# Optimization experiments

Hardware: AMD Instinct MI355X
Metric: run time of the kernel (lower is better)

The kernel has to match this reference:

```python
import jax, jax.numpy as jnp
import numpy as np

N_NODES = 50000
N_EDGES = 500000
HID = 128
NLAYERS = 4
NGRAPHS = 64
NODE_F = 15
EDGE_F = 3


def _init(key, shape, fan_in):
    return jax.random.normal(key, shape, dtype=jnp.float32) / np.sqrt(fan_in)


def setup_inputs() -> dict:
    key = jax.random.key(0)
    ks = jax.random.split(key, 32)
    inp = {}
    inp["x"] = jax.random.normal(ks[0], (N_NODES, NODE_F), dtype=jnp.float32)
    inp["edge_index"] = jax.random.randint(ks[1], (2, N_EDGES), 0, N_NODES, dtype=jnp.int64)
    inp["edge_attr"] = jax.random.normal(ks[2], (N_EDGES, EDGE_F), dtype=jnp.float32)
    inp["pos"] = jax.random.normal(ks[3], (N_NODES, 3), dtype=jnp.float32)
    inp["batch"] = jnp.sort(jax.random.randint(ks[4], (N_NODES,), 0, NGRAPHS, dtype=jnp.int64))
    # encoders
    inp["enc_w"] = _init(ks[5], (NODE_F, HID), NODE_F)
    inp["enc_b"] = jnp.zeros((HID,), jnp.float32)
    inp["eenc_w"] = _init(ks[6], (EDGE_F, HID), EDGE_F)
    inp["eenc_b"] = jnp.zeros((HID,), jnp.float32)
    # stacked per-layer conv params
    MIN = 2 * HID + 1  # message input dim = 257
    inp["msg_w1"] = _init(ks[7], (NLAYERS, MIN, HID), MIN)
    inp["msg_b1"] = jnp.zeros((NLAYERS, HID), jnp.float32)
    inp["msg_w2"] = _init(ks[8], (NLAYERS, HID, HID), HID)
    inp["msg_b2"] = jnp.zeros((NLAYERS, HID), jnp.float32)
    inp["upd_w1"] = _init(ks[9], (NLAYERS, 2 * HID, HID), 2 * HID)
    inp["upd_b1"] = jnp.zeros((NLAYERS, HID), jnp.float32)
    inp["upd_w2"] = _init(ks[10], (NLAYERS, HID, HID), HID)
    inp["upd_b2"] = jnp.zeros((NLAYERS, HID), jnp.float32)
    inp["ln_g"] = jnp.ones((NLAYERS, HID), jnp.float32)
    inp["ln_b"] = jnp.zeros((NLAYERS, HID), jnp.float32)
    # readout MLP (dropout is eval-mode identity)
    inp["mlp_w1"] = _init(ks[11], (HID, HID), HID)
    inp["mlp_b1"] = jnp.zeros((HID,), jnp.float32)
    inp["mlp_w2"] = _init(ks[12], (HID, HID // 2), HID)
    inp["mlp_b2"] = jnp.zeros((HID // 2,), jnp.float32)
    inp["mlp_w3"] = _init(ks[13], (HID // 2, 1), HID // 2)
    inp["mlp_b3"] = jnp.zeros((1,), jnp.float32)
    return inp


def reference(x, edge_index, edge_attr, pos, batch,
              enc_w, enc_b, eenc_w, eenc_b,
              msg_w1, msg_b1, msg_w2, msg_b2,
              upd_w1, upd_b1, upd_w2, upd_b2,
              ln_g, ln_b,
              mlp_w1, mlp_b1, mlp_w2, mlp_b2, mlp_w3, mlp_b3):
    n = x.shape[0]
    h = x @ enc_w + enc_b                      # [N, H] node encoder
    _ea = edge_attr @ eenc_w + eenc_b          # encoded but unused downstream (faithful to source)
    src = edge_index[0]                        # j (source)
    dst = edge_index[1]                        # i (target)
    dist = jnp.linalg.norm(pos[dst] - pos[src], axis=-1, keepdims=True)  # [E,1]
    for i in range(NLAYERS):
        xi = h[dst]
        xj = h[src]
        m_in = jnp.concatenate([xi, xj, dist], axis=-1)               # [E, 2H+1]
        m = jax.nn.relu(m_in @ msg_w1[i] + msg_b1[i]) @ msg_w2[i] + msg_b2[i]
        aggr = jax.ops.segment_sum(m, dst, num_segments=n)            # scatter-add -> [N,H]
        u_in = jnp.concatenate([h, aggr], axis=-1)                    # [N, 2H]
        u = jax.nn.relu(u_in @ upd_w1[i] + upd_b1[i]) @ upd_w2[i] + upd_b2[i]
        mu = jnp.mean(u, axis=-1, keepdims=True)
        var = jnp.mean((u - mu) ** 2, axis=-1, keepdims=True)
        u = (u - mu) / jnp.sqrt(var + 1e-5) * ln_g[i] + ln_b[i]
        u = jax.nn.relu(u)
        h = u if i == 0 else h + u
    # global mean pool over graphs
    cnt = jax.ops.segment_sum(jnp.ones((n, 1), h.dtype), batch, num_segments=NGRAPHS)
    pooled = jax.ops.segment_sum(h, batch, num_segments=NGRAPHS) / jnp.maximum(cnt, 1.0)
    o = jax.nn.relu(pooled @ mlp_w1 + mlp_b1)
    o = jax.nn.relu(o @ mlp_w2 + mlp_b2)
    return o @ mlp_w3 + mlp_b3                  # [NGRAPHS, 1]
```

## Files before the change

kernel.cpp:

```cpp
#include <hip/hip_runtime.h>
#include <hip/hip_bf16.h>
#include <cstdint>

#define N_NODES 50000
#define N_EDGES 500000
#define HID 128
#define NLAYERS 4
#define NGRAPHS 64
#define NTILES ((N_NODES + 63) / 64)
#define NPW 4
#define EBLOCKS ((N_NODES + NPW * 4 - 1) / (NPW * 4))

typedef float f32x4 __attribute__((ext_vector_type(4)));
typedef __bf16 bf16x8 __attribute__((ext_vector_type(8)));

__device__ float          g_h[(size_t)N_NODES * HID];
__device__ unsigned short g_hb[(size_t)N_NODES * HID];
__device__ float          g_S[(size_t)N_NODES * HID];
__device__ unsigned short g_PQ[(size_t)N_NODES * 256];
__device__ int2           g_edge[N_EDGES];
__device__ int            g_cnt[N_NODES];
__device__ int            g_cursor[N_NODES];
__device__ int            g_bsum[1024];
__device__ unsigned short g_pqw[NLAYERS * 4 * 16 * 64 * 8];
__device__ float          g_wc[NLAYERS * 128 * 128];
__device__ float          g_bc[NLAYERS * 128];
__device__ unsigned short g_uw1p[NLAYERS * 8 * 8 * 64 * 8];
__device__ unsigned short g_uw2p[NLAYERS * 4 * 8 * 64 * 8];
__device__ float          g_pooled[NGRAPHS * HID];

__device__ __forceinline__ unsigned short f2bf(float f) {
    uint32_t u = __builtin_bit_cast(uint32_t, f);
    uint32_t r = (u + 0x7fffu + ((u >> 16) & 1u)) >> 16;
    return (unsigned short)r;
}
__device__ __forceinline__ float bf2f(unsigned short u) {
    return __builtin_bit_cast(float, (uint32_t)u << 16);
}

__global__ void clear_cnt_k() {
    int i = blockIdx.x * 256 + threadIdx.x;
    if (i < N_NODES) g_cnt[i] = 0;
}
__global__ void clear_pooled_k() {
    int i = blockIdx.x * 256 + threadIdx.x;
    if (i < NGRAPHS * HID) g_pooled[i] = 0.f;
}

__global__ void pack_pqw_k(const float* __restrict__ w1) {
    int lane = threadIdx.x;
    int bid = blockIdx.x;
    int nt = bid & 15, ks = (bid >> 4) & 3, L = bid >> 6;
    const float* w = w1 + (size_t)L * 257 * HID;
    int kb = ks * 32 + (lane >> 4) * 8;
    int n = nt * 16 + (lane & 15);
    unsigned short tmp[8];
#pragma unroll
    for (int j = 0; j < 8; ++j) {
        int k = kb + j;
        float v = (n < 128) ? w[(size_t)k * HID + n] : w[(size_t)(128 + k) * HID + (n - 128)];
        tmp[j] = f2bf(v);
    }
    uint4 o = make_uint4(tmp[0] | ((uint32_t)tmp[1] << 16), tmp[2] | ((uint32_t)tmp[3] << 16),
                         tmp[4] | ((uint32_t)tmp[5] << 16), tmp[6] | ((uint32_t)tmp[7] << 16));
    *(uint4*)&g_pqw[(((size_t)(L * 4 + ks) * 16 + nt) * 64 + lane) * 8] = o;
}

__global__ void wc_k(const float* __restrict__ mw2, const float* __restrict__ uw1) {
    __shared__ float row[128];
    int L = blockIdx.x >> 7, k = blockIdx.x & 127, j = threadIdx.x;
    row[j] = mw2[(size_t)L * 128 * 128 + k * 128 + j];
    __syncthreads();
    const float* u1b = uw1 + (size_t)L * 256 * 128 + 128 * 128;
    float s = 0.f;
    for (int i = 0; i < 128; ++i) s += row[i] * u1b[i * 128 + j];
    g_wc[(size_t)L * 128 * 128 + k * 128 + j] = s;
}
__global__ void bc_k(const float* __restrict__ mb2, const float* __restrict__ uw1) {
    int L = blockIdx.x, j = threadIdx.x;
    const float* u1b = uw1 + (size_t)L * 256 * 128 + 128 * 128;
    const float* b2 = mb2 + L * 128;
    float s = 0.f;
    for (int i = 0; i < 128; ++i) s += b2[i] * u1b[i * 128 + j];
    g_bc[L * 128 + j] = s;
}

__global__ void pack_u1_k(const float* __restrict__ uw1) {
    int lane = threadIdx.x;
    int bid = blockIdx.x;
    int nt = bid & 7, ks = (bid >> 3) & 7, L = bid >> 6;
    int kb = ks * 32 + (lane >> 4) * 8;
    int n = nt * 16 + (lane & 15);
    unsigned short tmp[8];
#pragma unroll
    for (int j = 0; j < 8; ++j) {
        int k = kb + j;
        float v = (k < 128) ? uw1[(size_t)L * 256 * 128 + (size_t)k * 128 + n]
                            : g_wc[(size_t)L * 128 * 128 + (size_t)(k - 128) * 128 + n];
        tmp[j] = f2bf(v);
    }
    uint4 o = make_uint4(tmp[0] | ((uint32_t)tmp[1] << 16), tmp[2] | ((uint32_t)tmp[3] << 16),
                         tmp[4] | ((uint32_t)tmp[5] << 16), tmp[6] | ((uint32_t)tmp[7] << 16));
    *(uint4*)&g_uw1p[(((size_t)(L * 8 + ks) * 8 + nt) * 64 + lane) * 8] = o;
}

__global__ void pack_w2_k(const float* __restrict__ uw2) {
    int lane = threadIdx.x;
    int bid = blockIdx.x;
    int nt = bid & 7, ks = (bid >> 3) & 3, L = bid >> 5;
    int kb = ks * 32 + (lane >> 4) * 8;
    int n = nt * 16 + (lane & 15);
    unsigned short tmp[8];
#pragma unroll
    for (int j = 0; j < 8; ++j)
        tmp[j] = f2bf(uw2[(size_t)L * 128 * 128 + (size_t)(kb + j) * 128 + n]);
    uint4 o = make_uint4(tmp[0] | ((uint32_t)tmp[1] << 16), tmp[2] | ((uint32_t)tmp[3] << 16),
                         tmp[4] | ((uint32_t)tmp[5] << 16), tmp[6] | ((uint32_t)tmp[7] << 16));
    *(uint4*)&g_uw2p[(((size_t)(L * 4 + ks) * 8 + nt) * 64 + lane) * 8] = o;
}

__global__ void encode_k(const float* __restrict__ x, const float* __restrict__ w,
                         const float* __restrict__ b) {
    __shared__ float xl[2][15];
    int t = threadIdx.x;
    int half = t >> 7;
    int node = blockIdx.x * 2 + half;
    int c = t & 127;
    if (c < 15) xl[half][c] = x[(size_t)node * 15 + c];
    __syncthreads();
    float acc = b[c];
#pragma unroll
    for (int k = 0; k < 15; ++k) acc += xl[half][k] * w[k * HID + c];
    g_h[(size_t)node * HID + c] = acc;
    g_hb[(size_t)node * HID + c] = f2bf(acc);
}

__global__ void hist_k(const int* __restrict__ ei) {
    int e = blockIdx.x * 256 + threadIdx.x;
    if (e < N_EDGES) atomicAdd(&g_cnt[ei[N_EDGES + e]], 1);
}
__global__ void scanA_k() {
    __shared__ int s[512];
    int t = threadIdx.x;
    int i = blockIdx.x * 512 + t;
    s[t] = (i < N_NODES) ? g_cnt[i] : 0;
    __syncthreads();
    for (int d = 256; d > 0; d >>= 1) {
        if (t < d) s[t] += s[t + d];
        __syncthreads();
    }
    if (t == 0) g_bsum[blockIdx.x] = s[0];
}
__global__ void scanB_k(int nb) {
    if (threadIdx.x == 0) {
        int acc = 0;
        for (int i = 0; i < nb; ++i) { int v = g_bsum[i]; g_bsum[i] = acc; acc += v; }
    }
}
__global__ void scanC_k() {
    __shared__ int s[512];
    int t = threadIdx.x;
    int i = blockIdx.x * 512 + t;
    int v = (i < N_NODES) ? g_cnt[i] : 0;
    s[t] = v;
    __syncthreads();
    for (int d = 1; d < 512; d <<= 1) {
        int add = (t >= d) ? s[t - d] : 0;
        __syncthreads();
        s[t] += add;
        __syncthreads();
    }
    if (i < N_NODES) g_cursor[i] = g_bsum[blockIdx.x] + s[t] - v;
}
__global__ void scatter_k(const int* __restrict__ ei, const float* __restrict__ pos) {
    int e = blockIdx.x * 256 + threadIdx.x;
    if (e >= N_EDGES) return;
    int s = ei[e];
    int d = ei[N_EDGES + e];
    float dx = pos[d * 3 + 0] - pos[s * 3 + 0];
    float dy = pos[d * 3 + 1] - pos[s * 3 + 1];
    float dz = pos[d * 3 + 2] - pos[s * 3 + 2];
    float dist = sqrtf(dx * dx + dy * dy + dz * dz);
    int p = atomicAdd(&g_cursor[d], 1);
    g_edge[p] = make_int2(s, __builtin_bit_cast(int, dist));
}

__global__ __launch_bounds__(256, 2)
void pq_k(int L) {
    __shared__ unsigned short Abuf[64 * 128];
    __shared__ unsigned short Obuf[64 * 264];
    const unsigned short* wp = g_pqw + (size_t)L * 4 * 16 * 64 * 8;
    int t = threadIdx.x, wave = t >> 6, lane = t & 63;
    int arow = lane & 15, kgrp = lane >> 4;
    int tile0 = blockIdx.x * 64;

    {
        int r = t >> 2, p = t & 3;
        int n = tile0 + r;
        bool valid = n < N_NODES;
#pragma unroll
        for (int q = 0; q < 4; ++q) {
            int slot = p * 4 + q;
            uint4 v = make_uint4(0, 0, 0, 0);
            if (valid) v = *(const uint4*)&g_hb[(size_t)n * HID + slot * 8];
            *(uint4*)&Abuf[r * 128 + ((slot ^ (r & 7)) << 3)] = v;
        }
    }
    __syncthreads();

    bf16x8 wv[4][4];
#pragma unroll
    for (int ks = 0; ks < 4; ++ks)
#pragma unroll
        for (int ntl = 0; ntl < 4; ++ntl)
            wv[ks][ntl] = *(const bf16x8*)&wp[((size_t)(ks * 16 + wave * 4 + ntl) * 64 + lane) * 8];

    f32x4 acc[4][4];
#pragma unroll
    for (int rf = 0; rf < 4; ++rf)
#pragma unroll
        for (int ntl = 0; ntl < 4; ++ntl) acc[rf][ntl] = (f32x4){0.f, 0.f, 0.f, 0.f};
#pragma unroll
    for (int ks = 0; ks < 4; ++ks) {
        int slot = ks * 4 + kgrp;
#pragma unroll
        for (int rf = 0; rf < 4; ++rf) {
            int row = rf * 16 + arow;
            bf16x8 a = *(const bf16x8*)&Abuf[row * 128 + ((slot ^ (row & 7)) << 3)];
#pragma unroll
            for (int ntl = 0; ntl < 4; ++ntl)
                acc[rf][ntl] = __builtin_amdgcn_mfma_f32_16x16x32_bf16(a, wv[ks][ntl], acc[rf][ntl], 0, 0, 0);
        }
    }
#pragma unroll
    for (int rf = 0; rf < 4; ++rf)
#pragma unroll
        for (int ntl = 0; ntl < 4; ++ntl) {
            int col = wave * 64 + ntl * 16 + arow;
#pragma unroll
            for (int q = 0; q < 4; ++q) {
                int row = rf * 16 + kgrp * 4 + q;
                Obuf[row * 264 + col] = f2bf(acc[rf][ntl][q]);
            }
        }
    __syncthreads();
#pragma unroll
    for (int i = 0; i < 8; ++i) {
        int k = t + i * 256;
        int row = k >> 5, cc = k & 31;
        int n = tile0 + row;
        if (n < N_NODES)
            *(uint4*)&g_PQ[(size_t)n * 256 + cc * 8] = *(const uint4*)&Obuf[row * 264 + cc * 8];
    }
}

__global__ __launch_bounds__(256, 8)
void edge_relu_k(const float* __restrict__ w1last, const float* __restrict__ b1) {
    int t = threadIdx.x, wave = t >> 6, lane = t & 63;
    int c2 = lane * 2;
    float wl0 = w1last[c2], wl1 = w1last[c2 + 1];
    float bb0 = b1[c2], bb1 = b1[c2 + 1];

    int gw = blockIdx.x * 4 + wave;
    int n0 = gw * NPW;
    int n1 = n0 + NPW < N_NODES ? n0 + NPW : N_NODES;

    for (int n = n0; n < n1; ++n) {
        int end = g_cursor[n];
        int cnt = g_cnt[n];
        int beg = end - cnt;
        uint32_t pv = *(const uint32_t*)&g_PQ[(size_t)n * 256 + c2];
        float pb0 = bf2f((unsigned short)(pv & 0xffff)) + bb0;
        float pb1 = bf2f((unsigned short)(pv >> 16)) + bb1;
        float acc0 = 0.f, acc1 = 0.f;

        for (int cb = beg; cb < end; cb += 64) {
            int mye = cb + lane;
            bool v = mye < end;
            int2 ed = v ? g_edge[mye] : make_int2(0, 0);
            int msrc = ed.x;
            float mdist = __builtin_bit_cast(float, ed.y);
            int lim = end - cb < 64 ? end - cb : 64;
            int full = lim & ~7;
            for (int b = 0; b < full; b += 8) {
                uint32_t qv[8];
#pragma unroll
                for (int j = 0; j < 8; ++j) {
                    int s = __shfl(msrc, b + j);
                    qv[j] = *(const uint32_t*)&g_PQ[(size_t)s * 256 + 128 + c2];
                }
#pragma unroll
                for (int j = 0; j < 8; ++j) {
                    float dist = __shfl(mdist, b + j);
                    acc0 += fmaxf(fmaf(dist, wl0, pb0 + bf2f((unsigned short)(qv[j] & 0xffff))), 0.f);
                    acc1 += fmaxf(fmaf(dist, wl1, pb1 + bf2f((unsigned short)(qv[j] >> 16))), 0.f);
                }
            }
            for (int j = full; j < lim; ++j) {
                int s = __shfl(msrc, j);
                float dist = __shfl(mdist, j);
                uint32_t qv = *(const uint32_t*)&g_PQ[(size_t)s * 256 + 128 + c2];
                acc0 += fmaxf(fmaf(dist, wl0, pb0 + bf2f((unsigned short)(qv & 0xffff))), 0.f);
                acc1 += fmaxf(fmaf(dist, wl1, pb1 + bf2f((unsigned short)(qv >> 16))), 0.f);
            }
        }
        *(float2*)&g_S[(size_t)n * HID + c2] = make_float2(acc0, acc1);
    }
}

__global__ __launch_bounds__(256, 4)
void upd_k(const float* __restrict__ ub1, const float* __restrict__ ub2,
           const float* __restrict__ lng, const float* __restrict__ lnb,
           int L, int first_layer, int Lpq) {
    __shared__ unsigned short Abuf[64 * 128];
    __shared__ unsigned short Hbuf[64 * 128];
    __shared__ float rsums[2][2][64];
    __shared__ float degb[64];
    const unsigned short* w1p = g_uw1p + (size_t)L * 8 * 8 * 64 * 8;
    const unsigned short* w2p = g_uw2p + (size_t)L * 4 * 8 * 64 * 8;
    int t = threadIdx.x, wave = t >> 6, lane = t & 63;
    int wr = wave >> 1, wc = wave & 1;
    int arow = lane & 15, kgrp = lane >> 4;
    int tile0 = blockIdx.x * 64;

    int sr = t >> 2, sp = t & 3;
    int sn = tile0 + sr;
    bool svalid = sn < N_NODES;

    if (sp == 0) degb[sr] = svalid ? (float)g_cnt[sn] : 0.f;
#pragma unroll
    for (int q = 0; q < 4; ++q) {
        int slot = sp * 4 + q;
        uint4 v = make_uint4(0, 0, 0, 0);
        if (svalid) v = *(const uint4*)&g_hb[(size_t)sn * HID + slot * 8];
        *(uint4*)&Abuf[sr * 128 + ((slot ^ (sr & 7)) << 3)] = v;
    }
    __syncthreads();

    f32x4 acc0[4], acc1[4];
#pragma unroll
    for (int i = 0; i < 4; ++i) { acc0[i] = (f32x4){0.f,0.f,0.f,0.f}; acc1[i] = (f32x4){0.f,0.f,0.f,0.f}; }
    int r0 = wr * 32 + arow, r1 = r0 + 16;
#pragma unroll
    for (int ks = 0; ks < 4; ++ks) {
        int slot = ks * 4 + kgrp;
        bf16x8 a0 = *(const bf16x8*)&Abuf[r0 * 128 + ((slot ^ (arow & 7)) << 3)];
        bf16x8 a1 = *(const bf16x8*)&Abuf[r1 * 128 + ((slot ^ (arow & 7)) << 3)];
#pragma unroll
        for (int ntl = 0; ntl < 4; ++ntl) {
            bf16x8 b = *(const bf16x8*)&w1p[((size_t)(ks * 8 + wc * 4 + ntl) * 64 + lane) * 8];
            acc0[ntl] = __builtin_amdgcn_mfma_f32_16x16x32_bf16(a0, b, acc0[ntl], 0, 0, 0);
            acc1[ntl] = __builtin_amdgcn_mfma_f32_16x16x32_bf16(a1, b, acc1[ntl], 0, 0, 0);
        }
    }
    __syncthreads();

#pragma unroll
    for (int q = 0; q < 4; ++q) {
        int slot = sp * 4 + q;
        uint4 v = make_uint4(0, 0, 0, 0);
        if (svalid) {
            const float* spt = &g_S[(size_t)sn * HID + slot * 8];
            float4 f0 = *(const float4*)spt;
            float4 f1 = *((const float4*)spt + 1);
            v.x = f2bf(f0.x) | ((uint32_t)f2bf(f0.y) << 16);
            v.y = f2bf(f0.z) | ((uint32_t)f2bf(f0.w) << 16);
            v.z = f2bf(f1.x) | ((uint32_t)f2bf(f1.y) << 16);
            v.w = f2bf(f1.z) | ((uint32_t)f2bf(f1.w) << 16);
        }
        *(uint4*)&Abuf[sr * 128 + ((slot ^ (sr & 7)) << 3)] = v;
    }
    __syncthreads();

#pragma unroll
    for (int ks = 0; ks < 4; ++ks) {
        int slot = ks * 4 + kgrp;
        bf16x8 a0 = *(const bf16x8*)&Abuf[r0 * 128 + ((slot ^ (arow & 7)) << 3)];
        bf16x8 a1 = *(const bf16x8*)&Abuf[r1 * 128 + ((slot ^ (arow & 7)) << 3)];
#pragma unroll
        for (int ntl = 0; ntl < 4; ++ntl) {
            bf16x8 b = *(const bf16x8*)&w1p[((size_t)((ks + 4) * 8 + wc * 4 + ntl) * 64 + lane) * 8];
            acc0[ntl] = __builtin_amdgcn_mfma_f32_16x16x32_bf16(a0, b, acc0[ntl], 0, 0, 0);
            acc1[ntl] = __builtin_amdgcn_mfma_f32_16x16x32_bf16(a1, b, acc1[ntl], 0, 0, 0);
        }
    }

    float dg0[4], dg1[4];
#pragma unroll
    for (int q = 0; q < 4; ++q) {
        dg0[q] = degb[wr * 32 + kgrp * 4 + q];
        dg1[q] = degb[wr * 32 + 16 + kgrp * 4 + q];
    }
#pragma unroll
    for (int ntl = 0; ntl < 4; ++ntl) {
        int col = wc * 64 + ntl * 16 + arow;
        float bv1 = ub1[col], bcv = g_bc[L * 128 + col];
        int slotH = col >> 3, cl = col & 7;
#pragma unroll
        for (int q = 0; q < 4; ++q) {
            int rw0 = wr * 32 + kgrp * 4 + q;
            float h0 = fmaxf(acc0[ntl][q] + dg0[q] * bcv + bv1, 0.f);
            Hbuf[rw0 * 128 + ((slotH ^ (rw0 & 7)) << 3) + cl] = f2bf(h0);
            int rw1 = rw0 + 16;
            float h1 = fmaxf(acc1[ntl][q] + dg1[q] * bcv + bv1, 0.f);
            Hbuf[rw1 * 128 + ((slotH ^ (rw1 & 7)) << 3) + cl] = f2bf(h1);
        }
    }
    __syncthreads();

    f32x4 c0[4], c1[4];
#pragma unroll
    for (int i = 0; i < 4; ++i) { c0[i] = (f32x4){0.f,0.f,0.f,0.f}; c1[i] = (f32x4){0.f,0.f,0.f,0.f}; }
#pragma unroll
    for (int ks = 0; ks < 4; ++ks) {
        int slot = ks * 4 + kgrp;
        bf16x8 a0 = *(const bf16x8*)&Hbuf[r0 * 128 + ((slot ^ (arow & 7)) << 3)];
        bf16x8 a1 = *(const bf16x8*)&Hbuf[r1 * 128 + ((slot ^ (arow & 7)) << 3)];
#pragma unroll
        for (int ntl = 0; ntl < 4; ++ntl) {
            bf16x8 b = *(const bf16x8*)&w2p[((size_t)(ks * 8 + wc * 4 + ntl) * 64 + lane) * 8];
            c0[ntl] = __builtin_amdgcn_mfma_f32_16x16x32_bf16(a0, b, c0[ntl], 0, 0, 0);
            c1[ntl] = __builtin_amdgcn_mfma_f32_16x16x32_bf16(a1, b, c1[ntl], 0, 0, 0);
        }
    }

    float bv2[4], gm[4], bt[4];
#pragma unroll
    for (int ntl = 0; ntl < 4; ++ntl) {
        int col = wc * 64 + ntl * 16 + arow;
        bv2[ntl] = ub2[col]; gm[ntl] = lng[col]; bt[ntl] = lnb[col];
    }
    float s0[4] = {0,0,0,0}, s1[4] = {0,0,0,0}, q0[4] = {0,0,0,0}, q1[4] = {0,0,0,0};
#pragma unroll
    for (int ntl = 0; ntl < 4; ++ntl)
#pragma unroll
        for (int q = 0; q < 4; ++q) {
            float v0 = c0[ntl][q] + bv2[ntl];
            float v1 = c1[ntl][q] + bv2[ntl];
            c0[ntl][q] = v0; c1[ntl][q] = v1;
            s0[q] += v0; q0[q] += v0 * v0;
            s1[q] += v1; q1[q] += v1 * v1;
        }
#pragma unroll
    for (int m = 1; m < 16; m <<= 1)
#pragma unroll
        for (int q = 0; q < 4; ++q) {
            s0[q] += __shfl_xor(s0[q], m); q0[q] += __shfl_xor(q0[q], m);
            s1[q] += __shfl_xor(s1[q], m); q1[q] += __shfl_xor(q1[q], m);
        }
    if (arow == 0) {
#pragma unroll
        for (int q = 0; q < 4; ++q) {
            int rw0 = wr * 32 + kgrp * 4 + q;
            rsums[wc][0][rw0] = s0[q]; rsums[wc][1][rw0] = q0[q];
            rsums[wc][0][rw0 + 16] = s1[q]; rsums[wc][1][rw0 + 16] = q1[q];
        }
    }
    __syncthreads();

    float mean0[4], rstd0[4], mean1[4], rstd1[4];
#pragma unroll
    for (int q = 0; q < 4; ++q) {
        int rw0 = wr * 32 + kgrp * 4 + q;
        float sm = rsums[0][0][rw0] + rsums[1][0][rw0];
        float sq = rsums[0][1][rw0] + rsums[1][1][rw0];
        mean0[q] = sm * (1.f / HID);
        rstd0[q] = rsqrtf(sq * (1.f / HID) - mean0[q] * mean0[q] + 1e-5f);
        int rw1 = rw0 + 16;
        sm = rsums[0][0][rw1] + rsums[1][0][rw1];
        sq = rsums[0][1][rw1] + rsums[1][1][rw1];
        mean1[q] = sm * (1.f / HID);
        rstd1[q] = rsqrtf(sq * (1.f / HID) - mean1[q] * mean1[q] + 1e-5f);
    }

#pragma unroll
    for (int ntl = 0; ntl < 4; ++ntl) {
        int col = wc * 64 + ntl * 16 + arow;
        int slotA = col >> 3, clA = col & 7;
#pragma unroll
        for (int q = 0; q < 4; ++q) {
            int rw0 = wr * 32 + kgrp * 4 + q;
            int row0 = tile0 + rw0;
            float u0 = fmaxf((c0[ntl][q] - mean0[q]) * rstd0[q] * gm[ntl] + bt[ntl], 0.f);
            float hr0 = (!first_layer && row0 < N_NODES) ? g_h[(size_t)row0 * HID + col] : 0.f;
            float hn0 = first_layer ? u0 : (hr0 + u0);
            c0[ntl][q] = hn0;
            Abuf[rw0 * 128 + ((slotA ^ (rw0 & 7)) << 3) + clA] = f2bf(hn0);
            int rw1 = rw0 + 16;
            int row1 = row0 + 16;
            float u1 = fmaxf((c1[ntl][q] - mean1[q]) * rstd1[q] * gm[ntl] + bt[ntl], 0.f);
            float hr1 = (!first_layer && row1 < N_NODES) ? g_h[(size_t)row1 * HID + col] : 0.f;
            float hn1 = first_layer ? u1 : (hr1 + u1);
            c1[ntl][q] = hn1;
            Abuf[rw1 * 128 + ((slotA ^ (rw1 & 7)) << 3) + clA] = f2bf(hn1);
        }
    }
    __syncthreads();

    float* FB = (float*)Hbuf;
#pragma unroll
    for (int h = 0; h < 2; ++h) {
        if (wr == h) {
#pragma unroll
            for (int ntl = 0; ntl < 4; ++ntl) {
                int col = wc * 64 + ntl * 16 + arow;
#pragma unroll
                for (int q = 0; q < 4; ++q) {
                    int lr = kgrp * 4 + q;
                    FB[lr * 128 + col] = c0[ntl][q];
                    FB[(lr + 16) * 128 + col] = c1[ntl][q];
                }
            }
        }
        __syncthreads();
#pragma unroll
        for (int i = 0; i < 4; ++i) {
            int pos = t + i * 256;
            int row = pos >> 5, cc = pos & 31;
            int n = tile0 + h * 32 + row;
            if (n < N_NODES)
                *(float4*)&g_h[(size_t)n * HID + cc * 4] = *(const float4*)&FB[row * 128 + cc * 4];
        }
        __syncthreads();
    }

    if (Lpq < 0) return;

#pragma unroll
    for (int i = 0; i < 4; ++i) {
        int pos = t + i * 256;
        int row = pos >> 4, s = pos & 15;
        int n = tile0 + row;
        if (n < N_NODES)
            *(uint4*)&g_hb[(size_t)n * HID + s * 8] =
                *(const uint4*)&Abuf[row * 128 + ((s ^ (row & 7)) << 3)];
    }

    const unsigned short* wp = g_pqw + (size_t)Lpq * 4 * 16 * 64 * 8;
#pragma unroll
    for (int h = 0; h < 2; ++h) {
        bf16x8 w3[4][2];
#pragma unroll
        for (int ks = 0; ks < 4; ++ks)
#pragma unroll
            for (int j = 0; j < 2; ++j) {
                int nt = h * 8 + wave * 2 + j;
                w3[ks][j] = *(const bf16x8*)&wp[((size_t)(ks * 16 + nt) * 64 + lane) * 8];
            }
        f32x4 a3[4][2];
#pragma unroll
        for (int rf = 0; rf < 4; ++rf)
#pragma unroll
            for (int j = 0; j < 2; ++j) a3[rf][j] = (f32x4){0.f, 0.f, 0.f, 0.f};
#pragma unroll
        for (int ks = 0; ks < 4; ++ks) {
            int slot = ks * 4 + kgrp;
#pragma unroll
            for (int rf = 0; rf < 4; ++rf) {
                int row = rf * 16 + arow;
                bf16x8 a = *(const bf16x8*)&Abuf[row * 128 + ((slot ^ (arow & 7)) << 3)];
#pragma unroll
                for (int j = 0; j < 2; ++j)
                    a3[rf][j] = __builtin_amdgcn_mfma_f32_16x16x32_bf16(a, w3[ks][j], a3[rf][j], 0, 0, 0);
            }
        }
        __syncthreads();
#pragma unroll
        for (int rf = 0; rf < 4; ++rf)
#pragma unroll
            for (int j = 0; j < 2; ++j) {
                int cl2 = (wave * 2 + j) * 16 + arow;
                int slotP = cl2 >> 3, clP = cl2 & 7;
#pragma unroll
                for (int q = 0; q < 4; ++q) {
                    int row = rf * 16 + kgrp * 4 + q;
                    Hbuf[row * 128 + ((slotP ^ (row & 7)) << 3) + clP] = f2bf(a3[rf][j][q]);
                }
            }
        __syncthreads();
#pragma unroll
        for (int i = 0; i < 4; ++i) {
            int u = t + i * 256;
            int row = u >> 4, s = u & 15;
            int n2 = tile0 + row;
            if (n2 < N_NODES)
                *(uint4*)&g_PQ[(size_t)n2 * 256 + h * 128 + s * 8] =
                    *(const uint4*)&Hbuf[row * 128 + ((s ^ (row & 7)) << 3)];
        }
    }
}

__global__ __launch_bounds__(256, 8)
void pool_k(const int* __restrict__ batch) {
    __shared__ int se[2];
    __shared__ float part[2][128];
    int b = blockIdx.x;
    int g = b >> 3, sub = b & 7;
    int t = threadIdx.x;
    if (t == 0) {
        int lo = 0, hi = N_NODES;
        while (lo < hi) { int m = (lo + hi) >> 1; if (batch[m] < g) lo = m + 1; else hi = m; }
        se[0] = lo;
        hi = N_NODES;
        while (lo < hi) { int m = (lo + hi) >> 1; if (batch[m] < g + 1) lo = m + 1; else hi = m; }
        se[1] = lo;
    }
    __syncthreads();
    int s = se[0], e = se[1];
    int c = t & 127, half = t >> 7;
    float acc = 0.f;
    for (int n = s + sub * 2 + half; n < e; n += 16) acc += g_h[(size_t)n * HID + c];
    part[half][c] = acc;
    __syncthreads();
    if (t < 128) {
        float v = part[0][t] + part[1][t];
        atomicAdd(&g_pooled[g * HID + t], v);
    }
}

__global__ void readout_k(const int* __restrict__ batch,
                          const float* __restrict__ w1, const float* __restrict__ b1,
                          const float* __restrict__ w2, const float* __restrict__ b2,
                          const float* __restrict__ w3, const float* __restrict__ b3,
                          float* __restrict__ out) {
    __shared__ float p[128], o1[128], o2[64];
    __shared__ int se[2];
    int g = blockIdx.x, t = threadIdx.x;
    if (t == 0) {
        int lo = 0, hi = N_NODES;
        while (lo < hi) { int m = (lo + hi) >> 1; if (batch[m] < g) lo = m + 1; else hi = m; }
        se[0] = lo;
        hi = N_NODES;
        while (lo < hi) { int m = (lo + hi) >> 1; if (batch[m] < g + 1) lo = m + 1; else hi = m; }
        se[1] = lo;
    }
    __syncthreads();
    float cntf = fmaxf((float)(se[1] - se[0]), 1.f);
    p[t] = g_pooled[g * HID + t] / cntf;
    __syncthreads();
    float a = b1[t];
    for (int k = 0; k < 128; ++k) a += p[k] * w1[k * 128 + t];
    o1[t] = fmaxf(a, 0.f);
    __syncthreads();
    if (t < 64) {
        float a2 = b2[t];
        for (int k = 0; k < 128; ++k) a2 += o1[k] * w2[k * 64 + t];
        o2[t] = fmaxf(a2, 0.f);
    }
    __syncthreads();
    if (t == 0) {
        float a3 = b3[0];
        for (int k = 0; k < 64; ++k) a3 += o2[k] * w3[k];
        out[g] = a3;
    }
}

extern "C" void kernel_launch(void* const* d_in, const int* in_sizes, int n_in,
                              void* d_out, int out_size, void* d_ws, size_t ws_size,
                              hipStream_t stream) {
    const float* x     = (const float*)d_in[0];
    const int*   ei    = (const int*)d_in[1];
    const float* pos   = (const float*)d_in[3];
    const int*   batch = (const int*)d_in[4];
    const float* enc_w = (const float*)d_in[5];
    const float* enc_b = (const float*)d_in[6];
    const float* msg_w1 = (const float*)d_in[9];
    const float* msg_b1 = (const float*)d_in[10];
    const float* msg_w2 = (const float*)d_in[11];
    const float* msg_b2 = (const float*)d_in[12];
    const float* upd_w1 = (const float*)d_in[13];
    const float* upd_b1 = (const float*)d_in[14];
    const float* upd_w2 = (const float*)d_in[15];
    const float* upd_b2 = (const float*)d_in[16];
    const float* ln_g   = (const float*)d_in[17];
    const float* ln_b   = (const float*)d_in[18];
    const float* mw1 = (const float*)d_in[19];
    const float* mb1 = (const float*)d_in[20];
    const float* mw2 = (const float*)d_in[21];
    const float* mb2 = (const float*)d_in[22];
    const float* mw3 = (const float*)d_in[23];
    const float* mb3 = (const float*)d_in[24];
    float* out = (float*)d_out;
    (void)d_ws; (void)ws_size; (void)in_sizes; (void)n_in; (void)out_size;

    pack_pqw_k<<<NLAYERS * 4 * 16, 64, 0, stream>>>(msg_w1);
    wc_k<<<NLAYERS * 128, 128, 0, stream>>>(msg_w2, upd_w1);
    bc_k<<<NLAYERS, 128, 0, stream>>>(msg_b2, upd_w1);
    pack_u1_k<<<NLAYERS * 8 * 8, 64, 0, stream>>>(upd_w1);
    pack_w2_k<<<NLAYERS * 4 * 8, 64, 0, stream>>>(upd_w2);

    encode_k<<<N_NODES / 2, 256, 0, stream>>>(x, enc_w, enc_b);

    clear_cnt_k<<<(N_NODES + 255) / 256, 256, 0, stream>>>();
    hist_k<<<(N_EDGES + 255) / 256, 256, 0, stream>>>(ei);
    int nb = (N_NODES + 511) / 512;
    scanA_k<<<nb, 512, 0, stream>>>();
    scanB_k<<<1, 64, 0, stream>>>(nb);
    scanC_k<<<nb, 512, 0, stream>>>();
    scatter_k<<<(N_EDGES + 255) / 256, 256, 0, stream>>>(ei, pos);

    pq_k<<<NTILES, 256, 0, stream>>>(0);
    clear_pooled_k<<<32, 256, 0, stream>>>();
    for (int L = 0; L < NLAYERS; ++L) {
        edge_relu_k<<<EBLOCKS, 256, 0, stream>>>(
            msg_w1 + (size_t)L * 257 * HID + 256 * HID, msg_b1 + L * HID);
        upd_k<<<NTILES, 256, 0, stream>>>(
            upd_b1 + L * HID, upd_b2 + L * HID, ln_g + L * HID, ln_b + L * HID,
            L, L == 0 ? 1 : 0, L < NLAYERS - 1 ? L + 1 : -1);
    }

    pool_k<<<NGRAPHS * 8, 256, 0, stream>>>(batch);
    readout_k<<<NGRAPHS, 128, 0, stream>>>(batch, mw1, mb1, mw2, mb2, mw3, mb3, out);
}
```

Baseline: 554.1 us.

## Fuse node encoder into first PQ kernel, deepen gather batching, prefetch S

The standalone encoder kernel is folded into the layer-0 PQ projection, so the encoded tile is built directly in shared memory instead of being written out and read back. The edge aggregation loop now issues 16 independent gathers per batch instead of 8, exposing more memory-level parallelism at the cost of more registers. The update kernel loads its aggregated S rows at kernel start, so that latency overlaps the first GEMM phase. The added shared memory in the fused kernel and the extra registers could reduce occupancy.

```diff
diff --git a/kernel.cpp b/kernel.cpp
--- a/kernel.cpp
+++ b/kernel.cpp
@@ -119,22 +119,6 @@
     *(uint4*)&g_uw2p[(((size_t)(L * 4 + ks) * 8 + nt) * 64 + lane) * 8] = o;
 }
 
-__global__ void encode_k(const float* __restrict__ x, const float* __restrict__ w,
-                         const float* __restrict__ b) {
-    __shared__ float xl[2][15];
-    int t = threadIdx.x;
-    int half = t >> 7;
-    int node = blockIdx.x * 2 + half;
-    int c = t & 127;
-    if (c < 15) xl[half][c] = x[(size_t)node * 15 + c];
-    __syncthreads();
-    float acc = b[c];
-#pragma unroll
-    for (int k = 0; k < 15; ++k) acc += xl[half][k] * w[k * HID + c];
-    g_h[(size_t)node * HID + c] = acc;
-    g_hb[(size_t)node * HID + c] = f2bf(acc);
-}
-
 __global__ void hist_k(const int* __restrict__ ei) {
     int e = blockIdx.x * 256 + threadIdx.x;
     if (e < N_EDGES) atomicAdd(&g_cnt[ei[N_EDGES + e]], 1);
@@ -186,24 +170,40 @@
 }
 
 __global__ __launch_bounds__(256, 2)
-void pq_k(int L) {
+void encode_pq_k(const float* __restrict__ x, const float* __restrict__ ew,
+                 const float* __restrict__ eb) {
+    __shared__ float xl[64][16];
+    __shared__ float wenc[15][128];
     __shared__ unsigned short Abuf[64 * 128];
     __shared__ unsigned short Obuf[64 * 264];
-    const unsigned short* wp = g_pqw + (size_t)L * 4 * 16 * 64 * 8;
+    const unsigned short* wp = g_pqw;
     int t = threadIdx.x, wave = t >> 6, lane = t & 63;
     int arow = lane & 15, kgrp = lane >> 4;
     int tile0 = blockIdx.x * 64;
 
+    for (int i = t; i < 15 * 128; i += 256) wenc[i >> 7][i & 127] = ew[i];
+    for (int i = t; i < 64 * 15; i += 256) {
+        int r = i / 15, c = i % 15;
+        int n = tile0 + r;
+        xl[r][c] = (n < N_NODES) ? x[(size_t)n * 15 + c] : 0.f;
+    }
+    __syncthreads();
+
     {
-        int r = t >> 2, p = t & 3;
-        int n = tile0 + r;
-        bool valid = n < N_NODES;
-#pragma unroll
-        for (int q = 0; q < 4; ++q) {
-            int slot = p * 4 + q;
-            uint4 v = make_uint4(0, 0, 0, 0);
-            if (valid) v = *(const uint4*)&g_hb[(size_t)n * HID + slot * 8];
-            *(uint4*)&Abuf[r * 128 + ((slot ^ (r & 7)) << 3)] = v;
+        int c = t & 127, half = t >> 7;
+        float bb = eb[c];
+        int slot = c >> 3, cl = c & 7;
+        for (int rr = half; rr < 64; rr += 2) {
+            float acc = bb;
+#pragma unroll
+            for (int k = 0; k < 15; ++k) acc += xl[rr][k] * wenc[k][c];
+            unsigned short hb = f2bf(acc);
+            Abuf[rr * 128 + ((slot ^ (rr & 7)) << 3) + cl] = hb;
+            int n = tile0 + rr;
+            if (n < N_NODES) {
+                g_h[(size_t)n * HID + c] = acc;
+                g_hb[(size_t)n * HID + c] = hb;
+            }
         }
     }
     __syncthreads();
@@ -281,17 +281,17 @@
             int msrc = ed.x;
             float mdist = __builtin_bit_cast(float, ed.y);
             int lim = end - cb < 64 ? end - cb : 64;
-            int full = lim & ~7;
-            for (int b = 0; b < full; b += 8) {
-                uint32_t qv[8];
-#pragma unroll
-                for (int j = 0; j < 8; ++j) {
-                    int s = __shfl(msrc, b + j);
+            int full = lim & ~15;
+            for (int bq = 0; bq < full; bq += 16) {
+                uint32_t qv[16];
+#pragma unroll
+                for (int j = 0; j < 16; ++j) {
+                    int s = __shfl(msrc, bq + j);
                     qv[j] = *(const uint32_t*)&g_PQ[(size_t)s * 256 + 128 + c2];
                 }
 #pragma unroll
-                for (int j = 0; j < 8; ++j) {
-                    float dist = __shfl(mdist, b + j);
+                for (int j = 0; j < 16; ++j) {
+                    float dist = __shfl(mdist, bq + j);
                     acc0 += fmaxf(fmaf(dist, wl0, pb0 + bf2f((unsigned short)(qv[j] & 0xffff))), 0.f);
                     acc1 += fmaxf(fmaf(dist, wl1, pb1 + bf2f((unsigned short)(qv[j] >> 16))), 0.f);
                 }
@@ -327,6 +327,18 @@
     int sn = tile0 + sr;
     bool svalid = sn < N_NODES;
 
+    float4 sv0[4], sv1[4];
+#pragma unroll
+    for (int q = 0; q < 4; ++q) {
+        sv0[q] = make_float4(0.f, 0.f, 0.f, 0.f);
+        sv1[q] = make_float4(0.f, 0.f, 0.f, 0.f);
+        if (svalid) {
+            const float* spt = &g_S[(size_t)sn * HID + (sp * 4 + q) * 8];
+            sv0[q] = *(const float4*)spt;
+            sv1[q] = *((const float4*)spt + 1);
+        }
+    }
+
     if (sp == 0) degb[sr] = svalid ? (float)g_cnt[sn] : 0.f;
 #pragma unroll
     for (int q = 0; q < 4; ++q) {
@@ -358,16 +370,11 @@
 #pragma unroll
     for (int q = 0; q < 4; ++q) {
         int slot = sp * 4 + q;
-        uint4 v = make_uint4(0, 0, 0, 0);
-        if (svalid) {
-            const float* spt = &g_S[(size_t)sn * HID + slot * 8];
-            float4 f0 = *(const float4*)spt;
-            float4 f1 = *((const float4*)spt + 1);
-            v.x = f2bf(f0.x) | ((uint32_t)f2bf(f0.y) << 16);
-            v.y = f2bf(f0.z) | ((uint32_t)f2bf(f0.w) << 16);
-            v.z = f2bf(f1.x) | ((uint32_t)f2bf(f1.y) << 16);
-            v.w = f2bf(f1.z) | ((uint32_t)f2bf(f1.w) << 16);
-        }
+        uint4 v;
+        v.x = f2bf(sv0[q].x) | ((uint32_t)f2bf(sv0[q].y) << 16);
+        v.y = f2bf(sv0[q].z) | ((uint32_t)f2bf(sv0[q].w) << 16);
+        v.z = f2bf(sv1[q].x) | ((uint32_t)f2bf(sv1[q].y) << 16);
+        v.w = f2bf(sv1[q].z) | ((uint32_t)f2bf(sv1[q].w) << 16);
         *(uint4*)&Abuf[sr * 128 + ((slot ^ (sr & 7)) << 3)] = v;
     }
     __syncthreads();
@@ -689,8 +696,6 @@
     pack_u1_k<<<NLAYERS * 8 * 8, 64, 0, stream>>>(upd_w1);
     pack_w2_k<<<NLAYERS * 4 * 8, 64, 0, stream>>>(upd_w2);
 
-    encode_k<<<N_NODES / 2, 256, 0, stream>>>(x, enc_w, enc_b);
-
     clear_cnt_k<<<(N_NODES + 255) / 256, 256, 0, stream>>>();
     hist_k<<<(N_EDGES + 255) / 256, 256, 0, stream>>>(ei);
     int nb = (N_NODES + 511) / 512;
@@ -699,7 +704,7 @@
     scanC_k<<<nb, 512, 0, stream>>>();
     scatter_k<<<(N_EDGES + 255) / 256, 256, 0, stream>>>(ei, pos);
 
-    pq_k<<<NTILES, 256, 0, stream>>>(0);
+    encode_pq_k<<<NTILES, 256, 0, stream>>>(x, enc_w, enc_b);
     clear_pooled_k<<<32, 256, 0, stream>>>();
     for (int L = 0; L < NLAYERS; ++L) {
         edge_relu_k<<<EBLOCKS, 256, 0, stream>>>(
```

Result: slower. 614.8 us (+11.0%).
